# Performance work log

Hardware: AMD Instinct MI355X
Metric: run time of the kernel (lower is better)

The kernel has to match this reference:

```python
import jax, jax.numpy as jnp
import numpy as np

TOP_K = 2
LOGIT_SCALE = 1.0


def setup_inputs() -> dict:
    key = jax.random.key(0)
    k = jax.random.split(key, 5)
    B, S, C = 1, 1024, 1024
    E, I = 8, 1024           # experts, per-expert intermediate
    x = jax.random.normal(k[0], (B, S, C), dtype=jnp.float32)
    router_w = jax.random.normal(k[1], (E, C), dtype=jnp.float32) * 0.02
    w_in = jax.random.normal(k[2], (E, 2 * I, C), dtype=jnp.float32) * 0.02
    b_in = jnp.zeros((E, 2 * I), dtype=jnp.float32)
    w_out = jax.random.normal(k[3], (E, C, I), dtype=jnp.float32) * 0.02
    b_out = jnp.zeros((E, C), dtype=jnp.float32)
    return {"x": x, "router_w": router_w, "w_in": w_in, "b_in": b_in,
            "w_out": w_out, "b_out": b_out}


def reference(x, router_w, w_in, b_in, w_out, b_out):
    B, S, C = x.shape
    E = router_w.shape[0]
    xt = x.reshape(-1, C)                               # [T, C] flattened tokens
    T = xt.shape[0]

    # Router: softmax over all experts, then top-k probs as combine weights.
    logits = (xt @ router_w.T) * LOGIT_SCALE            # [T, E]
    probs = jax.nn.softmax(logits, axis=-1)
    top_w, top_idx = jax.lax.top_k(probs, TOP_K)        # [T, K]

    # Sparse gate matrix: nonzero only at the top-k experts per token.
    gate = jnp.zeros((T, E), dtype=probs.dtype)
    gate = gate.at[jnp.arange(T)[:, None], top_idx].set(top_w)  # [T, E]

    # Expert SwiGLU MLP, dense over experts, masked combine by gate.
    h = jnp.einsum('tc,eoc->teo', xt, w_in) + b_in      # [T, E, 2I]
    g, u = jnp.split(h, 2, axis=-1)                     # gate / input halves
    a = jax.nn.silu(g) * u                              # swiglu  [T, E, I]
    y = jnp.einsum('tei,eci->tec', a, w_out) + b_out    # [T, E, C]
    out = jnp.einsum('te,tec->tc', gate, y)             # combine top-k experts
    return out.reshape(B, S, C)
```

## Files before the change

kernel.cpp:

```cpp
#include <hip/hip_runtime.h>
#include <hip/hip_bf16.h>
#include <stdint.h>

#define TTOK 1024
#define CDIM 1024
#define NEXP 8
#define IDIM 1024
#define TWOI 2048
#define NSLOT 2048
#define NSTEP 16

typedef float f32x4 __attribute__((ext_vector_type(4)));
typedef short s16x8 __attribute__((ext_vector_type(8)));
typedef unsigned short u16;
typedef u16 u16x4 __attribute__((ext_vector_type(4)));
typedef u16 u16x8 __attribute__((ext_vector_type(8)));

#define VMCNT(n) asm volatile("s_waitcnt vmcnt(" #n ")" ::: "memory")
#define SBAR() __builtin_amdgcn_s_barrier()
#define SCHED0() __builtin_amdgcn_sched_barrier(0)

__device__ __forceinline__ u16 f2bf(float f) {
  unsigned x = __float_as_uint(f);
  x += 0x7fffu + ((x >> 16) & 1u);
  return (u16)(x >> 16);
}

__device__ __forceinline__ void gload_lds16(const void* g, void* l) {
  __builtin_amdgcn_global_load_lds(
      (const __attribute__((address_space(1))) void*)g,
      (__attribute__((address_space(3))) void*)l, 16, 0, 0);
}

__global__ __launch_bounds__(256) void cvtw_k(const float* __restrict__ win,
                                              const float* __restrict__ wout,
                                              u16* __restrict__ bin,
                                              u16* __restrict__ bout) {
  const int NIN = NEXP * TWOI * CDIM;
  const int NTOT = NIN + NEXP * CDIM * IDIM;
  for (int i = (blockIdx.x * 256 + threadIdx.x) * 8; i < NTOT;
       i += gridDim.x * 256 * 8) {
    const float* src;
    u16* dst;
    int j;
    if (i < NIN) { src = win; dst = bin; j = i; }
    else         { src = wout; dst = bout; j = i - NIN; }
    f32x4 v0 = *(const f32x4*)(src + j);
    f32x4 v1 = *(const f32x4*)(src + j + 4);
    u16x8 o;
#pragma unroll
    for (int q = 0; q < 4; ++q) o[q] = f2bf(v0[q]);
#pragma unroll
    for (int q = 0; q < 4; ++q) o[4 + q] = f2bf(v1[q]);
    *(u16x8*)(dst + j) = o;
  }
}

__global__ __launch_bounds__(64) void router_k(const float* __restrict__ x,
                                               const float* __restrict__ rw,
                                               float* __restrict__ topw,
                                               int* __restrict__ topidx,
                                               u16* __restrict__ xb) {
  const int t = blockIdx.x;
  const int lane = threadIdx.x;
  float p[NEXP];
#pragma unroll
  for (int e = 0; e < NEXP; ++e) p[e] = 0.f;
  const float* xr = x + (size_t)t * CDIM;
  u16* xbr = xb + (size_t)t * CDIM;
  for (int c0 = lane * 4; c0 < CDIM; c0 += 64 * 4) {
    f32x4 xv = *(const f32x4*)(xr + c0);
    u16x4 xc;
#pragma unroll
    for (int q = 0; q < 4; ++q) xc[q] = f2bf(xv[q]);
    *(u16x4*)(xbr + c0) = xc;
#pragma unroll
    for (int e = 0; e < NEXP; ++e) {
      f32x4 wv = *(const f32x4*)(rw + (size_t)e * CDIM + c0);
      p[e] += xv[0] * wv[0] + xv[1] * wv[1] + xv[2] * wv[2] + xv[3] * wv[3];
    }
  }
#pragma unroll
  for (int e = 0; e < NEXP; ++e) {
    float v = p[e];
#pragma unroll
    for (int off = 32; off >= 1; off >>= 1) v += __shfl_xor(v, off);
    p[e] = v;
  }
  if (lane == 0) {
    float m = p[0];
#pragma unroll
    for (int e = 1; e < NEXP; ++e) m = fmaxf(m, p[e]);
    float pe[NEXP];
    float den = 0.f;
#pragma unroll
    for (int e = 0; e < NEXP; ++e) { pe[e] = __expf(p[e] - m); den += pe[e]; }
    int i0 = 0;
#pragma unroll
    for (int e = 1; e < NEXP; ++e) if (p[e] > p[i0]) i0 = e;
    int i1 = (i0 == 0) ? 1 : 0;
#pragma unroll
    for (int e = 0; e < NEXP; ++e) if (e != i0 && p[e] > p[i1]) i1 = e;
    const float inv = 1.f / den;
    topw[t * 2] = pe[i0] * inv;
    topw[t * 2 + 1] = pe[i1] * inv;
    topidx[t * 2] = i0;
    topidx[t * 2 + 1] = i1;
  }
}

__global__ __launch_bounds__(1024) void build_k(const int* __restrict__ topidx,
                                                const float* __restrict__ topw,
                                                int* __restrict__ meta,
                                                int* __restrict__ slot_token,
                                                float* __restrict__ gatew) {
  __shared__ int cnt[NEXP], off[NEXP], cur[NEXP];
  const int t = threadIdx.x;
  if (t < NEXP) { cnt[t] = 0; cur[t] = 0; }
  __syncthreads();
  const int e0 = topidx[t * 2];
  const int e1 = topidx[t * 2 + 1];
  atomicAdd(&cnt[e0], 1);
  atomicAdd(&cnt[e1], 1);
  __syncthreads();
  if (t == 0) {
    int acc = 0;
    for (int e = 0; e < NEXP; ++e) { off[e] = acc; acc += cnt[e]; }
  }
  __syncthreads();
  if (t < NEXP) { meta[t] = cnt[t]; meta[16 + t] = off[t]; }
  {
    const int p0 = atomicAdd(&cur[e0], 1);
    const int s0 = off[e0] + p0;
    slot_token[s0] = t;
    gatew[s0] = topw[t * 2];
    const int p1 = atomicAdd(&cur[e1], 1);
    const int s1 = off[e1] + p1;
    slot_token[s1] = t;
    gatew[s1] = topw[t * 2 + 1];
  }
}

__global__ __launch_bounds__(256) void gemm1_k(const u16* __restrict__ A,
                                               const u16* __restrict__ Wb,
                                               const float* __restrict__ b_in,
                                               u16* __restrict__ Aout,
                                               const int* __restrict__ meta,
                                               const int* __restrict__ slot_token) {
  constexpr int BM = 128, K = CDIM;
  const int e = blockIdx.z;
  const int cnt = meta[e];
  const int m0 = blockIdx.y * BM;
  if (m0 >= cnt) return;
  const int off = meta[16 + e];
  const int i0 = blockIdx.x * 32;

  __shared__ u16 sA[3][BM * 64];
  __shared__ u16 sB[3][64 * 64];

  const int tid = threadIdx.x;
  const int lane = tid & 63;
  const int w = tid >> 6;
  const int wr = w >> 1;
  const int wc = w & 1;

  const u16* aSrc[4];
  int aDst[4];
#pragma unroll
  for (int i = 0; i < 4; ++i) {
    const int r = w * 32 + i * 8 + (lane >> 3);
    int rr = m0 + r;
    if (rr > cnt - 1) rr = cnt - 1;
    const int rowg = slot_token[off + rr];
    const int cs = (lane & 7) ^ (r & 7);
    aSrc[i] = A + (size_t)rowg * K + cs * 8;
    aDst[i] = (w * 32 + i * 8) * 64 + lane * 8;
  }
  const u16* bSrc[2];
  int bDst[2];
#pragma unroll
  for (int i = 0; i < 2; ++i) {
    const int r = w * 16 + i * 8 + (lane >> 3);
    const int wrow = (r & 1) ? (IDIM + i0 + (r >> 1)) : (i0 + (r >> 1));
    const int cs = (lane & 7) ^ (r & 7);
    bSrc[i] = Wb + ((size_t)e * TWOI + wrow) * K + cs * 8;
    bDst[i] = (w * 16 + i * 8) * 64 + lane * 8;
  }

  f32x4 acc[4][2];
#pragma unroll
  for (int m = 0; m < 4; ++m)
#pragma unroll
    for (int n = 0; n < 2; ++n) acc[m][n] = (f32x4){0.f, 0.f, 0.f, 0.f};

  auto STAGE = [&](int t) {
    const int cb = t % 3;
    const int ko = t * 64;
#pragma unroll
    for (int i = 0; i < 4; ++i) gload_lds16(aSrc[i] + ko, &sA[cb][aDst[i]]);
#pragma unroll
    for (int i = 0; i < 2; ++i) gload_lds16(bSrc[i] + ko, &sB[cb][bDst[i]]);
  };
  auto COMPUTE = [&](int cb) {
#pragma unroll
    for (int kh = 0; kh < 2; ++kh) {
      const int j = kh * 4 + (lane >> 4);
      s16x8 af[4], bf[2];
#pragma unroll
      for (int m = 0; m < 4; ++m) {
        const int r = wr * 64 + m * 16 + (lane & 15);
        af[m] = *(const s16x8*)(&sA[cb][r * 64 + ((j ^ (r & 7)) * 8)]);
      }
#pragma unroll
      for (int n = 0; n < 2; ++n) {
        const int r = wc * 32 + n * 16 + (lane & 15);
        bf[n] = *(const s16x8*)(&sB[cb][r * 64 + ((j ^ (r & 7)) * 8)]);
      }
#pragma unroll
      for (int m = 0; m < 4; ++m)
#pragma unroll
        for (int n = 0; n < 2; ++n)
          acc[m][n] = __builtin_amdgcn_mfma_f32_16x16x32_bf16(af[m], bf[n], acc[m][n], 0, 0, 0);
    }
  };

  STAGE(0);
  STAGE(1);
  for (int t = 0; t < NSTEP - 2; ++t) {
    STAGE(t + 2);
    VMCNT(12); SCHED0();
    SBAR();
    COMPUTE(t % 3);
    SBAR();
  }
  VMCNT(6); SCHED0(); SBAR(); COMPUTE((NSTEP - 2) % 3); SBAR();
  VMCNT(0); SCHED0(); SBAR(); COMPUTE((NSTEP - 1) % 3);

#pragma unroll
  for (int m = 0; m < 4; ++m) {
#pragma unroll
    for (int jj = 0; jj < 4; ++jj) {
      const int tr = wr * 64 + m * 16 + ((lane >> 4) * 4) + jj;
      const bool live = (m0 + tr) < cnt;
      const size_t slot = (size_t)(off + m0 + tr);
#pragma unroll
      for (int n = 0; n < 2; ++n) {
        const int cc = wc * 32 + n * 16 + (lane & 15);
        const int wrow_c = (cc & 1) ? (IDIM + i0 + (cc >> 1)) : (i0 + (cc >> 1));
        float v = acc[m][n][jj] + b_in[(size_t)e * TWOI + wrow_c];
        const float vo = __shfl_xor(v, 1);
        if (!(lane & 1) && live) {
          const float g = v, u = vo;
          const float aval = (g / (1.f + __expf(-g))) * u;
          Aout[slot * IDIM + i0 + (cc >> 1)] = f2bf(aval);
        }
      }
    }
  }
}

__global__ __launch_bounds__(256) void gemm2_k(const u16* __restrict__ A,
                                               const u16* __restrict__ Wb,
                                               const float* __restrict__ b_out,
                                               float* __restrict__ out,
                                               const int* __restrict__ meta,
                                               const int* __restrict__ slot_token,
                                               const float* __restrict__ gatew) {
  constexpr int BM = 64, K = IDIM;
  const int e = blockIdx.z;
  const int cnt = meta[e];
  const int m0 = blockIdx.y * BM;
  if (m0 >= cnt) return;
  const int off = meta[16 + e];
  const int n0 = blockIdx.x * 64;

  __shared__ u16 sA[3][BM * 64];
  __shared__ u16 sB[3][64 * 64];

  const int tid = threadIdx.x;
  const int lane = tid & 63;
  const int w = tid >> 6;
  const int wr = w >> 1;
  const int wc = w & 1;

  const u16* aSrc[2];
  int aDst[2];
#pragma unroll
  for (int i = 0; i < 2; ++i) {
    const int r = w * 16 + i * 8 + (lane >> 3);
    int rr = m0 + r;
    if (rr > cnt - 1) rr = cnt - 1;
    const int cs = (lane & 7) ^ (r & 7);
    aSrc[i] = A + (size_t)(off + rr) * K + cs * 8;
    aDst[i] = (w * 16 + i * 8) * 64 + lane * 8;
  }
  const u16* bSrc[2];
  int bDst[2];
#pragma unroll
  for (int i = 0; i < 2; ++i) {
    const int r = w * 16 + i * 8 + (lane >> 3);
    const int cs = (lane & 7) ^ (r & 7);
    bSrc[i] = Wb + ((size_t)e * CDIM + (n0 + r)) * K + cs * 8;
    bDst[i] = (w * 16 + i * 8) * 64 + lane * 8;
  }

  f32x4 acc[2][2];
#pragma unroll
  for (int m = 0; m < 2; ++m)
#pragma unroll
    for (int n = 0; n < 2; ++n) acc[m][n] = (f32x4){0.f, 0.f, 0.f, 0.f};

  auto STAGE = [&](int t) {
    const int cb = t % 3;
    const int ko = t * 64;
#pragma unroll
    for (int i = 0; i < 2; ++i) gload_lds16(aSrc[i] + ko, &sA[cb][aDst[i]]);
#pragma unroll
    for (int i = 0; i < 2; ++i) gload_lds16(bSrc[i] + ko, &sB[cb][bDst[i]]);
  };
  auto COMPUTE = [&](int cb) {
#pragma unroll
    for (int kh = 0; kh < 2; ++kh) {
      const int j = kh * 4 + (lane >> 4);
      s16x8 af[2], bf[2];
#pragma unroll
      for (int m = 0; m < 2; ++m) {
        const int r = wr * 32 + m * 16 + (lane & 15);
        af[m] = *(const s16x8*)(&sA[cb][r * 64 + ((j ^ (r & 7)) * 8)]);
      }
#pragma unroll
      for (int n = 0; n < 2; ++n) {
        const int r = wc * 32 + n * 16 + (lane & 15);
        bf[n] = *(const s16x8*)(&sB[cb][r * 64 + ((j ^ (r & 7)) * 8)]);
      }
#pragma unroll
      for (int m = 0; m < 2; ++m)
#pragma unroll
        for (int n = 0; n < 2; ++n)
          acc[m][n] = __builtin_amdgcn_mfma_f32_16x16x32_bf16(af[m], bf[n], acc[m][n], 0, 0, 0);
    }
  };

  STAGE(0);
  STAGE(1);
  for (int t = 0; t < NSTEP - 2; ++t) {
    STAGE(t + 2);
    VMCNT(8); SCHED0();
    SBAR();
    COMPUTE(t % 3);
    SBAR();
  }
  VMCNT(4); SCHED0(); SBAR(); COMPUTE((NSTEP - 2) % 3); SBAR();
  VMCNT(0); SCHED0(); SBAR(); COMPUTE((NSTEP - 1) % 3);

#pragma unroll
  for (int m = 0; m < 2; ++m) {
#pragma unroll
    for (int jj = 0; jj < 4; ++jj) {
      const int tr = wr * 32 + m * 16 + ((lane >> 4) * 4) + jj;
      if (m0 + tr < cnt) {
        const int slot = off + m0 + tr;
        const int tok = slot_token[slot];
        const float gw = gatew[slot];
#pragma unroll
        for (int n = 0; n < 2; ++n) {
          const int col = n0 + wc * 32 + n * 16 + (lane & 15);
          const float v = acc[m][n][jj] + b_out[(size_t)e * CDIM + col];
          atomicAdd(&out[(size_t)tok * CDIM + col], gw * v);
        }
      }
    }
  }
}

extern "C" void kernel_launch(void* const* d_in, const int* in_sizes, int n_in,
                              void* d_out, int out_size, void* d_ws, size_t ws_size,
                              hipStream_t stream) {
  const float* x = (const float*)d_in[0];
  const float* rw = (const float*)d_in[1];
  const float* w_in = (const float*)d_in[2];
  const float* b_in = (const float*)d_in[3];
  const float* w_out = (const float*)d_in[4];
  const float* b_out = (const float*)d_in[5];
  float* out = (float*)d_out;
  char* ws = (char*)d_ws;

  int* meta = (int*)ws;
  int* slot_token = (int*)(ws + 1024);
  float* topw = (float*)(ws + 1024 + 8192);
  int* topidx = (int*)(ws + 1024 + 16384);
  float* gatew = (float*)(ws + 1024 + 24576);
  u16* xb = (u16*)(ws + 65536);
  u16* a = (u16*)(ws + 65536 + (2u << 20));
  u16* wbin = (u16*)(ws + 65536 + (6u << 20));
  u16* wbout = (u16*)(ws + 65536 + (38u << 20));

  hipMemsetAsync(out, 0, (size_t)TTOK * CDIM * sizeof(float), stream);
  cvtw_k<<<2048, 256, 0, stream>>>(w_in, w_out, wbin, wbout);
  router_k<<<TTOK, 64, 0, stream>>>(x, rw, topw, topidx, xb);
  build_k<<<1, 1024, 0, stream>>>(topidx, topw, meta, slot_token, gatew);
  gemm1_k<<<dim3(32, 16, NEXP), 256, 0, stream>>>(
      xb, wbin, b_in, a, meta, slot_token);
  gemm2_k<<<dim3(16, 32, NEXP), 256, 0, stream>>>(
      a, wbout, b_out, out, meta, slot_token, gatew);
}
```

Before: 192.8 us.

## Fuse weight conversion, routing, slot build and output zeroing into one prep kernel

Merges the weight bf16 conversion, the router, the single-block slot builder and the output memset into one multi-role kernel, split by block index. Slot assignment now uses global atomics into fixed per-expert capacity regions (expert*1024) instead of a prefix-sum layout. This removes several launches and the serialized single-block build step. In exchange, slot order within an expert becomes nondeterministic, the workspace layout grows, and the GEMM grids shrink to match the per-expert capacity.

Result: slower. 205.5 us (+6.6%).

```diff
diff --git a/kernel.cpp b/kernel.cpp
--- a/kernel.cpp
+++ b/kernel.cpp
@@ -7,7 +7,7 @@
 #define NEXP 8
 #define IDIM 1024
 #define TWOI 2048
-#define NSLOT 2048
+#define CAP 1024
 #define NSTEP 16
 
 typedef float f32x4 __attribute__((ext_vector_type(4)));
@@ -32,112 +32,90 @@
       (__attribute__((address_space(3))) void*)l, 16, 0, 0);
 }
 
-__global__ __launch_bounds__(256) void cvtw_k(const float* __restrict__ win,
-                                              const float* __restrict__ wout,
-                                              u16* __restrict__ bin,
-                                              u16* __restrict__ bout) {
-  const int NIN = NEXP * TWOI * CDIM;
-  const int NTOT = NIN + NEXP * CDIM * IDIM;
-  for (int i = (blockIdx.x * 256 + threadIdx.x) * 8; i < NTOT;
-       i += gridDim.x * 256 * 8) {
-    const float* src;
-    u16* dst;
-    int j;
-    if (i < NIN) { src = win; dst = bin; j = i; }
-    else         { src = wout; dst = bout; j = i - NIN; }
-    f32x4 v0 = *(const f32x4*)(src + j);
-    f32x4 v1 = *(const f32x4*)(src + j + 4);
-    u16x8 o;
-#pragma unroll
-    for (int q = 0; q < 4; ++q) o[q] = f2bf(v0[q]);
-#pragma unroll
-    for (int q = 0; q < 4; ++q) o[4 + q] = f2bf(v1[q]);
-    *(u16x8*)(dst + j) = o;
-  }
-}
-
-__global__ __launch_bounds__(64) void router_k(const float* __restrict__ x,
-                                               const float* __restrict__ rw,
-                                               float* __restrict__ topw,
-                                               int* __restrict__ topidx,
-                                               u16* __restrict__ xb) {
-  const int t = blockIdx.x;
-  const int lane = threadIdx.x;
-  float p[NEXP];
-#pragma unroll
-  for (int e = 0; e < NEXP; ++e) p[e] = 0.f;
-  const float* xr = x + (size_t)t * CDIM;
-  u16* xbr = xb + (size_t)t * CDIM;
-  for (int c0 = lane * 4; c0 < CDIM; c0 += 64 * 4) {
-    f32x4 xv = *(const f32x4*)(xr + c0);
-    u16x4 xc;
-#pragma unroll
-    for (int q = 0; q < 4; ++q) xc[q] = f2bf(xv[q]);
-    *(u16x4*)(xbr + c0) = xc;
+__global__ __launch_bounds__(256) void prep_k(const float* __restrict__ x,
+                                              const float* __restrict__ rw,
+                                              const float* __restrict__ w_in,
+                                              const float* __restrict__ w_out,
+                                              u16* __restrict__ xb,
+                                              u16* __restrict__ wbin,
+                                              u16* __restrict__ wbout,
+                                              int* __restrict__ meta,
+                                              int* __restrict__ slot_token,
+                                              float* __restrict__ gatew,
+                                              float* __restrict__ out) {
+  const int bid = blockIdx.x;
+  const int tid = threadIdx.x;
+  if (bid < 2048) {
+    const int NIN = NEXP * TWOI * CDIM;
+    const int NTOT = NIN + NEXP * CDIM * IDIM;
+    for (int i = (bid * 256 + tid) * 8; i < NTOT; i += 2048 * 256 * 8) {
+      const float* src;
+      u16* dst;
+      int j;
+      if (i < NIN) { src = w_in; dst = wbin; j = i; }
+      else         { src = w_out; dst = wbout; j = i - NIN; }
+      f32x4 v0 = *(const f32x4*)(src + j);
+      f32x4 v1 = *(const f32x4*)(src + j + 4);
+      u16x8 o;
+#pragma unroll
+      for (int q = 0; q < 4; ++q) o[q] = f2bf(v0[q]);
+#pragma unroll
+      for (int q = 0; q < 4; ++q) o[4 + q] = f2bf(v1[q]);
+      *(u16x8*)(dst + j) = o;
+    }
+  } else if (bid < 2304) {
+    const int t = (bid - 2048) * 4 + (tid >> 6);
+    const int lane = tid & 63;
+    float p[NEXP];
+#pragma unroll
+    for (int e = 0; e < NEXP; ++e) p[e] = 0.f;
+    const float* xr = x + (size_t)t * CDIM;
+    u16* xbr = xb + (size_t)t * CDIM;
+    for (int c0 = lane * 4; c0 < CDIM; c0 += 256) {
+      f32x4 xv = *(const f32x4*)(xr + c0);
+      u16x4 xc;
+#pragma unroll
+      for (int q = 0; q < 4; ++q) xc[q] = f2bf(xv[q]);
+      *(u16x4*)(xbr + c0) = xc;
+#pragma unroll
+      for (int e = 0; e < NEXP; ++e) {
+        f32x4 wv = *(const f32x4*)(rw + (size_t)e * CDIM + c0);
+        p[e] += xv[0] * wv[0] + xv[1] * wv[1] + xv[2] * wv[2] + xv[3] * wv[3];
+      }
+    }
 #pragma unroll
     for (int e = 0; e < NEXP; ++e) {
-      f32x4 wv = *(const f32x4*)(rw + (size_t)e * CDIM + c0);
-      p[e] += xv[0] * wv[0] + xv[1] * wv[1] + xv[2] * wv[2] + xv[3] * wv[3];
-    }
-  }
-#pragma unroll
-  for (int e = 0; e < NEXP; ++e) {
-    float v = p[e];
-#pragma unroll
-    for (int off = 32; off >= 1; off >>= 1) v += __shfl_xor(v, off);
-    p[e] = v;
-  }
-  if (lane == 0) {
-    float m = p[0];
-#pragma unroll
-    for (int e = 1; e < NEXP; ++e) m = fmaxf(m, p[e]);
-    float pe[NEXP];
-    float den = 0.f;
-#pragma unroll
-    for (int e = 0; e < NEXP; ++e) { pe[e] = __expf(p[e] - m); den += pe[e]; }
-    int i0 = 0;
-#pragma unroll
-    for (int e = 1; e < NEXP; ++e) if (p[e] > p[i0]) i0 = e;
-    int i1 = (i0 == 0) ? 1 : 0;
-#pragma unroll
-    for (int e = 0; e < NEXP; ++e) if (e != i0 && p[e] > p[i1]) i1 = e;
-    const float inv = 1.f / den;
-    topw[t * 2] = pe[i0] * inv;
-    topw[t * 2 + 1] = pe[i1] * inv;
-    topidx[t * 2] = i0;
-    topidx[t * 2 + 1] = i1;
-  }
-}
-
-__global__ __launch_bounds__(1024) void build_k(const int* __restrict__ topidx,
-                                                const float* __restrict__ topw,
-                                                int* __restrict__ meta,
-                                                int* __restrict__ slot_token,
-                                                float* __restrict__ gatew) {
-  __shared__ int cnt[NEXP], off[NEXP], cur[NEXP];
-  const int t = threadIdx.x;
-  if (t < NEXP) { cnt[t] = 0; cur[t] = 0; }
-  __syncthreads();
-  const int e0 = topidx[t * 2];
-  const int e1 = topidx[t * 2 + 1];
-  atomicAdd(&cnt[e0], 1);
-  atomicAdd(&cnt[e1], 1);
-  __syncthreads();
-  if (t == 0) {
-    int acc = 0;
-    for (int e = 0; e < NEXP; ++e) { off[e] = acc; acc += cnt[e]; }
-  }
-  __syncthreads();
-  if (t < NEXP) { meta[t] = cnt[t]; meta[16 + t] = off[t]; }
-  {
-    const int p0 = atomicAdd(&cur[e0], 1);
-    const int s0 = off[e0] + p0;
-    slot_token[s0] = t;
-    gatew[s0] = topw[t * 2];
-    const int p1 = atomicAdd(&cur[e1], 1);
-    const int s1 = off[e1] + p1;
-    slot_token[s1] = t;
-    gatew[s1] = topw[t * 2 + 1];
+      float v = p[e];
+#pragma unroll
+      for (int off = 32; off >= 1; off >>= 1) v += __shfl_xor(v, off);
+      p[e] = v;
+    }
+    if (lane == 0) {
+      float m = p[0];
+#pragma unroll
+      for (int e = 1; e < NEXP; ++e) m = fmaxf(m, p[e]);
+      float pe[NEXP];
+      float den = 0.f;
+#pragma unroll
+      for (int e = 0; e < NEXP; ++e) { pe[e] = __expf(p[e] - m); den += pe[e]; }
+      int i0 = 0;
+#pragma unroll
+      for (int e = 1; e < NEXP; ++e) if (p[e] > p[i0]) i0 = e;
+      int i1 = (i0 == 0) ? 1 : 0;
+#pragma unroll
+      for (int e = 0; e < NEXP; ++e) if (e != i0 && p[e] > p[i1]) i1 = e;
+      const float inv = 1.f / den;
+      const int p0 = atomicAdd(&meta[i0], 1);
+      slot_token[i0 * CAP + p0] = t;
+      gatew[i0 * CAP + p0] = pe[i0] * inv;
+      const int p1 = atomicAdd(&meta[i1], 1);
+      slot_token[i1 * CAP + p1] = t;
+      gatew[i1 * CAP + p1] = pe[i1] * inv;
+    }
+  } else {
+    for (int i = ((bid - 2304) * 256 + tid) * 4; i < TTOK * CDIM;
+         i += 256 * 256 * 4)
+      *(f32x4*)(out + i) = (f32x4){0.f, 0.f, 0.f, 0.f};
   }
 }
 
@@ -152,7 +130,7 @@
   const int cnt = meta[e];
   const int m0 = blockIdx.y * BM;
   if (m0 >= cnt) return;
-  const int off = meta[16 + e];
+  const int off = e * CAP;
   const int i0 = blockIdx.x * 32;
 
   __shared__ u16 sA[3][BM * 64];
@@ -271,7 +249,7 @@
   const int cnt = meta[e];
   const int m0 = blockIdx.y * BM;
   if (m0 >= cnt) return;
-  const int off = meta[16 + e];
+  const int off = e * CAP;
   const int n0 = blockIdx.x * 64;
 
   __shared__ u16 sA[3][BM * 64];
@@ -387,20 +365,17 @@
 
   int* meta = (int*)ws;
   int* slot_token = (int*)(ws + 1024);
-  float* topw = (float*)(ws + 1024 + 8192);
-  int* topidx = (int*)(ws + 1024 + 16384);
-  float* gatew = (float*)(ws + 1024 + 24576);
-  u16* xb = (u16*)(ws + 65536);
-  u16* a = (u16*)(ws + 65536 + (2u << 20));
-  u16* wbin = (u16*)(ws + 65536 + (6u << 20));
-  u16* wbout = (u16*)(ws + 65536 + (38u << 20));
-
-  hipMemsetAsync(out, 0, (size_t)TTOK * CDIM * sizeof(float), stream);
-  cvtw_k<<<2048, 256, 0, stream>>>(w_in, w_out, wbin, wbout);
-  router_k<<<TTOK, 64, 0, stream>>>(x, rw, topw, topidx, xb);
-  build_k<<<1, 1024, 0, stream>>>(topidx, topw, meta, slot_token, gatew);
-  gemm1_k<<<dim3(32, 16, NEXP), 256, 0, stream>>>(
+  float* gatew = (float*)(ws + 1024 + 32768);
+  u16* xb = (u16*)(ws + 131072);
+  u16* a = (u16*)(ws + 131072 + (2u << 20));
+  u16* wbin = (u16*)(ws + 131072 + (18u << 20));
+  u16* wbout = (u16*)(ws + 131072 + (50u << 20));
+
+  hipMemsetAsync(meta, 0, 128, stream);
+  prep_k<<<2560, 256, 0, stream>>>(x, rw, w_in, w_out, xb, wbin, wbout,
+                                   meta, slot_token, gatew, out);
+  gemm1_k<<<dim3(32, 8, NEXP), 256, 0, stream>>>(
       xb, wbin, b_in, a, meta, slot_token);
-  gemm2_k<<<dim3(16, 32, NEXP), 256, 0, stream>>>(
+  gemm2_k<<<dim3(16, 16, NEXP), 256, 0, stream>>>(
       a, wbout, b_out, out, meta, slot_token, gatew);
 }
```
